# Performance work log

Measured on AMD Instinct MI355X. Metric: run time of the kernel, lower is better.

Reference implementation:

```python
import jax, jax.numpy as jnp
import numpy as np

N_NODES = 50000
N_EDGES = 600000
IN_DIM = 128
HID_DIM = 128


def setup_inputs() -> dict:
    key = jax.random.key(0)
    k_h, k_src, k_dst, k_w1, k_b1, k_w2, k_b2 = jax.random.split(key, 7)
    h = jax.random.normal(k_h, (N_NODES, IN_DIM), dtype=jnp.float32)
    src = jax.random.randint(k_src, (N_EDGES,), 0, N_NODES, dtype=jnp.int32)
    dst = jax.random.randint(k_dst, (N_EDGES,), 0, N_NODES, dtype=jnp.int32)
    # Edge MLP params: Linear(in_dim, out_dim) -> ReLU -> Linear(out_dim, 1) -> ReLU
    s1 = 1.0 / np.sqrt(IN_DIM)
    s2 = 1.0 / np.sqrt(HID_DIM)
    W1 = jax.random.uniform(k_w1, (IN_DIM, HID_DIM), jnp.float32, -s1, s1)
    b1 = jax.random.uniform(k_b1, (HID_DIM,), jnp.float32, -s1, s1)
    W2 = jax.random.uniform(k_w2, (HID_DIM, 1), jnp.float32, -s2, s2)
    b2 = jax.random.uniform(k_b2, (1,), jnp.float32, -s2, s2)
    return {"h": h, "src": src, "dst": dst, "W1": W1, "b1": b1, "W2": W2, "b2": b2}


def reference(h, src, dst, W1, b1, W2, b2):
    n_nodes = h.shape[0]
    # Edge MLP on feature differences (gather src/dst node features)
    dif = h[src] - h[dst]                                   # [E, D]
    hidden = jax.nn.relu(dif @ W1 + b1)                      # [E, H]
    att = jax.nn.relu(hidden @ W2 + b2)[:, 0]                # [E]
    att = jax.nn.sigmoid(att)                                # [E]
    # EdgeWeightNorm('right') on reversed graph: divide by the sum of
    # attention weights over edges sharing the same ORIGINAL source node.
    denom = jax.ops.segment_sum(att, src, num_segments=n_nodes)  # [N]
    w = att / denom[src]                                     # [E]
    # Message: w_e * src features, sum-aggregated at destination nodes
    msg = w[:, None] * h[src]                                # [E, D]
    out = jax.ops.segment_sum(msg, dst, num_segments=n_nodes)  # [N, D]
    return out
```

## Files before the change

### kernel.cpp

```cpp
#include <hip/hip_runtime.h>


typedef unsigned int uint;
typedef unsigned short ushort;
typedef __attribute__((ext_vector_type(8))) short short8;
typedef __attribute__((ext_vector_type(4))) float f32x4;

static __device__ __forceinline__ uint pack_f16(float a, float b) {
  _Float16 ha = (_Float16)a, hb = (_Float16)b;
  unsigned short ua = __builtin_bit_cast(unsigned short, ha);
  unsigned short ub = __builtin_bit_cast(unsigned short, hb);
  return ((uint)ub << 16) | ua;
}
static __device__ __forceinline__ float2 unpack_f16(uint u) {
  _Float16 lo = __builtin_bit_cast(_Float16, (unsigned short)(u & 0xffffu));
  _Float16 hi = __builtin_bit_cast(_Float16, (unsigned short)(u >> 16));
  return make_float2((float)lo, (float)hi);
}
static __device__ __forceinline__ ushort f2bf(float x) {
  uint u = __float_as_uint(x);
  u += 0x7fffu + ((u >> 16) & 1u);
  return (ushort)(u >> 16);
}

__global__ __launch_bounds__(256) void k_transpose(const float* __restrict__ W1,
                                                   ushort* __restrict__ w1t_swz) {
  int idx = blockIdx.x * 256 + threadIdx.x;
  int n = idx >> 7, k = idx & 127;
  float v = W1[k * 128 + n];
  int byte_off = n * 256 + ((k * 2) ^ ((n & 7) << 4));
  w1t_swz[byte_off >> 1] = f2bf(v);
}

__global__ __launch_bounds__(256) void k_gemm(const float* __restrict__ h,
                                              const ushort* __restrict__ w1t_swz,
                                              uint* __restrict__ gh,
                                              uint4* __restrict__ hh4,
                                              int n_nodes) {
  __shared__ ushort w1s[16384];
  int tid = threadIdx.x;
  {
    const uint4* srcw = (const uint4*)w1t_swz;
    uint4* dstw = (uint4*)w1s;
    #pragma unroll
    for (int i = 0; i < 8; ++i) dstw[tid + 256 * i] = srcw[tid + 256 * i];
  }
  __syncthreads();
  int wave = tid >> 6, lane = tid & 63;
  int tile = blockIdx.x * 4 + wave;
  if (tile * 16 >= n_nodes) return;
  int n0 = tile * 16;
  int l15 = lane & 15, kq = lane >> 4;
  int row = n0 + l15;

  f32x4 acc[8];
  #pragma unroll
  for (int ct = 0; ct < 8; ++ct) acc[ct] = (f32x4){0.f, 0.f, 0.f, 0.f};

  #pragma unroll
  for (int kb = 0; kb < 4; ++kb) {
    const float* hp = &h[(size_t)row * 128 + kb * 32 + kq * 8];
    float4 p0 = *(const float4*)hp;
    float4 p1 = *(const float4*)(hp + 4);
    short8 a;
    a[0] = (short)f2bf(p0.x); a[1] = (short)f2bf(p0.y);
    a[2] = (short)f2bf(p0.z); a[3] = (short)f2bf(p0.w);
    a[4] = (short)f2bf(p1.x); a[5] = (short)f2bf(p1.y);
    a[6] = (short)f2bf(p1.z); a[7] = (short)f2bf(p1.w);
    uint4 hv;
    hv.x = pack_f16(p0.x, p0.y); hv.y = pack_f16(p0.z, p0.w);
    hv.z = pack_f16(p1.x, p1.y); hv.w = pack_f16(p1.z, p1.w);
    hh4[(size_t)row * 16 + kb * 4 + kq] = hv;
    #pragma unroll
    for (int ct = 0; ct < 8; ++ct) {
      int n = ct * 16 + l15;
      int byte_off = n * 256 + (((kb * 64) + kq * 16) ^ ((n & 7) << 4));
      short8 b = *(const short8*)((const char*)w1s + byte_off);
      acc[ct] = __builtin_amdgcn_mfma_f32_16x16x32_bf16(a, b, acc[ct], 0, 0, 0);
    }
  }
  ushort* gh16 = (ushort*)gh;
  #pragma unroll
  for (int ct = 0; ct < 8; ++ct) {
    #pragma unroll
    for (int r = 0; r < 4; ++r) {
      int orow = n0 + kq * 4 + r;
      _Float16 v = (_Float16)acc[ct][r];
      gh16[(size_t)orow * 128 + ct * 16 + l15] = __builtin_bit_cast(unsigned short, v);
    }
  }
}

__global__ __launch_bounds__(256) void k_att(const uint4* __restrict__ gh4,
                                             const int* __restrict__ src,
                                             const int* __restrict__ dst,
                                             const float* __restrict__ b1,
                                             const float* __restrict__ W2,
                                             const float* __restrict__ b2,
                                             float* __restrict__ att,
                                             float* __restrict__ denom,
                                             int* __restrict__ counts,
                                             int n_edges) {
  int lane = threadIdx.x & 63;
  int sub = lane >> 4, l16 = lane & 15;
  int wid = (int)((blockIdx.x * blockDim.x + threadIdx.x) >> 6);
  int gw = (int)((gridDim.x * blockDim.x) >> 6);
  float4 b1a = *(const float4*)&b1[l16 * 8];
  float4 b1b = *(const float4*)&b1[l16 * 8 + 4];
  float4 w2a = *(const float4*)&W2[l16 * 8];
  float4 w2b = *(const float4*)&W2[l16 * 8 + 4];
  float b2v = b2[0];
  for (int e0 = wid * 4; e0 < n_edges; e0 += gw * 4) {
    int e = e0 + sub;
    bool valid = e < n_edges;
    int s = 0, d = 0;
    float acc = 0.f;
    if (valid) {
      s = src[e];
      d = dst[e];
      uint4 us = gh4[(size_t)s * 16 + l16];
      uint4 ud = gh4[(size_t)d * 16 + l16];
      float2 s0 = unpack_f16(us.x), s1 = unpack_f16(us.y);
      float2 s2 = unpack_f16(us.z), s3 = unpack_f16(us.w);
      float2 d0 = unpack_f16(ud.x), d1 = unpack_f16(ud.y);
      float2 d2 = unpack_f16(ud.z), d3 = unpack_f16(ud.w);
      float t;
      t = fmaxf(s0.x - d0.x + b1a.x, 0.f); acc = fmaf(t, w2a.x, acc);
      t = fmaxf(s0.y - d0.y + b1a.y, 0.f); acc = fmaf(t, w2a.y, acc);
      t = fmaxf(s1.x - d1.x + b1a.z, 0.f); acc = fmaf(t, w2a.z, acc);
      t = fmaxf(s1.y - d1.y + b1a.w, 0.f); acc = fmaf(t, w2a.w, acc);
      t = fmaxf(s2.x - d2.x + b1b.x, 0.f); acc = fmaf(t, w2b.x, acc);
      t = fmaxf(s2.y - d2.y + b1b.y, 0.f); acc = fmaf(t, w2b.y, acc);
      t = fmaxf(s3.x - d3.x + b1b.z, 0.f); acc = fmaf(t, w2b.z, acc);
      t = fmaxf(s3.y - d3.y + b1b.w, 0.f); acc = fmaf(t, w2b.w, acc);
    }
    acc += __shfl_xor(acc, 1);
    acc += __shfl_xor(acc, 2);
    acc += __shfl_xor(acc, 4);
    acc += __shfl_xor(acc, 8);
    if (l16 == 0 && valid) {
      float a = fmaxf(acc + b2v, 0.f);
      a = 1.f / (1.f + __expf(-a));
      att[e] = a;
      atomicAdd(&denom[s], a);
      atomicAdd(&counts[d], 1);
    }
  }
}

__global__ __launch_bounds__(256) void k_scanA(const int* __restrict__ counts,
                                               int* __restrict__ partials,
                                               int n, int chunk) {
  __shared__ int red[256];
  int b = blockIdx.x, t = threadIdx.x;
  int idx = b * chunk + t;
  red[t] = (t < chunk && idx < n) ? counts[idx] : 0;
  __syncthreads();
  for (int off = 128; off > 0; off >>= 1) {
    if (t < off) red[t] += red[t + off];
    __syncthreads();
  }
  if (t == 0) partials[b] = red[0];
}

__global__ __launch_bounds__(256) void k_scanB(int* __restrict__ partials,
                                               int* __restrict__ row_start,
                                               int n, int total) {
  __shared__ int p[256];
  int t = threadIdx.x;
  int orig = partials[t];
  p[t] = orig;
  __syncthreads();
  #pragma unroll
  for (int off = 1; off < 256; off <<= 1) {
    int v = (t >= off) ? p[t - off] : 0;
    __syncthreads();
    p[t] += v;
    __syncthreads();
  }
  partials[t] = p[t] - orig;
  if (t == 0) row_start[n] = total;
}

__global__ __launch_bounds__(256) void k_scanC(int* __restrict__ counts,
                                               const int* __restrict__ partials,
                                               int* __restrict__ row_start,
                                               int n, int chunk) {
  __shared__ int p[256];
  int b = blockIdx.x, t = threadIdx.x;
  int idx = b * chunk + t;
  bool ok = (t < chunk && idx < n);
  int orig = ok ? counts[idx] : 0;
  p[t] = orig;
  __syncthreads();
  #pragma unroll
  for (int off = 1; off < 256; off <<= 1) {
    int v = (t >= off) ? p[t - off] : 0;
    __syncthreads();
    p[t] += v;
    __syncthreads();
  }
  if (ok) {
    row_start[idx] = partials[b] + p[t] - orig;
    counts[idx] = 0;
  }
}

__global__ __launch_bounds__(256) void k_fill(const int* __restrict__ src,
                                              const int* __restrict__ dst,
                                              const float* __restrict__ att,
                                              const float* __restrict__ denom,
                                              const int* __restrict__ row_start,
                                              int* __restrict__ cursor,
                                              int2* __restrict__ bucket,
                                              int n_edges) {
  int i = blockIdx.x * blockDim.x + threadIdx.x;
  int stride = gridDim.x * blockDim.x;
  for (int e = i; e < n_edges; e += stride) {
    int d = dst[e], s = src[e];
    float w = att[e] / denom[s];
    int pos = atomicAdd(&cursor[d], 1);
    bucket[row_start[d] + pos] = make_int2(s, __float_as_int(w));
  }
}

__global__ __launch_bounds__(256) void k_agg(const uint4* __restrict__ hh4,
                                             const int* __restrict__ row_start,
                                             const int2* __restrict__ bucket,
                                             float* __restrict__ out, int n_nodes) {
  int lane = threadIdx.x & 63;
  int sub = lane >> 4, l16 = lane & 15;
  int d = blockIdx.x * 4 + (threadIdx.x >> 6);
  if (d >= n_nodes) return;
  int beg = row_start[d], end = row_start[d + 1];
  int cnt = end - beg;
  float a0 = 0.f, a1 = 0.f, a2 = 0.f, a3 = 0.f;
  float a4 = 0.f, a5 = 0.f, a6 = 0.f, a7 = 0.f;
  for (int base = 0; base < cnt; base += 64) {
    int nb = cnt - base; if (nb > 64) nb = 64;
    int2 ew = make_int2(0, 0);
    if (lane < nb) ew = bucket[beg + base + lane];
    int steps = (nb + 3) >> 2;
    for (int j = 0; j < steps; ++j) {
      int idx = j * 4 + sub;
      int s = __shfl(ew.x, idx);
      float w = __int_as_float(__shfl(ew.y, idx));
      if (idx < nb) {
        uint4 v = hh4[(size_t)s * 16 + l16];
        float2 f0 = unpack_f16(v.x), f1 = unpack_f16(v.y);
        float2 f2 = unpack_f16(v.z), f3 = unpack_f16(v.w);
        a0 = fmaf(w, f0.x, a0); a1 = fmaf(w, f0.y, a1);
        a2 = fmaf(w, f1.x, a2); a3 = fmaf(w, f1.y, a3);
        a4 = fmaf(w, f2.x, a4); a5 = fmaf(w, f2.y, a5);
        a6 = fmaf(w, f3.x, a6); a7 = fmaf(w, f3.y, a7);
      }
    }
  }
  #pragma unroll
  for (int off = 16; off < 64; off <<= 1) {
    a0 += __shfl_xor(a0, off); a1 += __shfl_xor(a1, off);
    a2 += __shfl_xor(a2, off); a3 += __shfl_xor(a3, off);
    a4 += __shfl_xor(a4, off); a5 += __shfl_xor(a5, off);
    a6 += __shfl_xor(a6, off); a7 += __shfl_xor(a7, off);
  }
  if (sub == 0) {
    *(float4*)&out[(size_t)d * 128 + l16 * 8]     = make_float4(a0, a1, a2, a3);
    *(float4*)&out[(size_t)d * 128 + l16 * 8 + 4] = make_float4(a4, a5, a6, a7);
  }
}

extern "C" void kernel_launch(void* const* d_in, const int* in_sizes, int n_in,
                              void* d_out, int out_size, void* d_ws, size_t ws_size,
                              hipStream_t stream) {
  const float* h   = (const float*)d_in[0];
  const int*   src = (const int*)d_in[1];
  const int*   dst = (const int*)d_in[2];
  const float* W1  = (const float*)d_in[3];
  const float* b1  = (const float*)d_in[4];
  const float* W2  = (const float*)d_in[5];
  const float* b2  = (const float*)d_in[6];
  float* out = (float*)d_out;

  int n_nodes = in_sizes[0] / 128;
  int n_edges = in_sizes[1];

  char* ws = (char*)d_ws;
  uint*   gh        = (uint*)ws;
  uint*   hh        = gh + (size_t)n_nodes * 64;
  float*  att       = (float*)(hh + (size_t)n_nodes * 64);
  float*  denom     = att + n_edges;
  int*    counts    = (int*)(denom + n_nodes);
  int*    row_start = counts + n_nodes;
  int*    partials  = row_start + n_nodes + 1;
  ushort* w1t       = (ushort*)(partials + 256);
  int2*   bucket    = (int2*)(((uintptr_t)(w1t + 16384) + 15) & ~(uintptr_t)15);

  hipMemsetAsync(denom, 0, (size_t)2 * n_nodes * sizeof(float), stream);

  int chunk = (n_nodes + 255) / 256;
  int n_tiles = (n_nodes + 15) / 16;
  k_transpose<<<64, 256, 0, stream>>>(W1, w1t);
  k_gemm <<<(n_tiles + 3) / 4, 256, 0, stream>>>(h, w1t, gh, (uint4*)hh, n_nodes);
  k_att  <<<2048, 256, 0, stream>>>((const uint4*)gh, src, dst, b1, W2, b2,
                                    att, denom, counts, n_edges);
  k_scanA<<<256, 256, 0, stream>>>(counts, partials, n_nodes, chunk);
  k_scanB<<<1, 256, 0, stream>>>(partials, row_start, n_nodes, n_edges);
  k_scanC<<<256, 256, 0, stream>>>(counts, partials, row_start, n_nodes, chunk);
  k_fill <<<2048, 256, 0, stream>>>(src, dst, att, denom, row_start, counts, bucket, n_edges);
  k_agg  <<<(n_nodes + 3) / 4, 256, 0, stream>>>((const uint4*)hh, row_start, bucket, out, n_nodes);
}
```

Before: 152.1 us.

## Compute edge attention in dst-sorted CSR order, reusing dst features per node

Builds the dst-bucketed CSR (histogram, scan, fill of source ids) before attention, then computes attention per destination node so the dst feature row and bias offsets are loaded once per node, not once per edge. Attention values go straight into the bucket array, and a separate pass then divides by the per-source denominator. This removes the per-edge dst gather and the att array round trip. It adds two extra launches (histogram and normalize) plus an extra pass over the bucket, and may load-imbalance on high-degree nodes.

```diff
diff --git a/kernel.cpp b/kernel.cpp
--- a/kernel.cpp
+++ b/kernel.cpp
@@ -91,61 +91,11 @@
   }
 }
 
-__global__ __launch_bounds__(256) void k_att(const uint4* __restrict__ gh4,
-                                             const int* __restrict__ src,
-                                             const int* __restrict__ dst,
-                                             const float* __restrict__ b1,
-                                             const float* __restrict__ W2,
-                                             const float* __restrict__ b2,
-                                             float* __restrict__ att,
-                                             float* __restrict__ denom,
-                                             int* __restrict__ counts,
-                                             int n_edges) {
-  int lane = threadIdx.x & 63;
-  int sub = lane >> 4, l16 = lane & 15;
-  int wid = (int)((blockIdx.x * blockDim.x + threadIdx.x) >> 6);
-  int gw = (int)((gridDim.x * blockDim.x) >> 6);
-  float4 b1a = *(const float4*)&b1[l16 * 8];
-  float4 b1b = *(const float4*)&b1[l16 * 8 + 4];
-  float4 w2a = *(const float4*)&W2[l16 * 8];
-  float4 w2b = *(const float4*)&W2[l16 * 8 + 4];
-  float b2v = b2[0];
-  for (int e0 = wid * 4; e0 < n_edges; e0 += gw * 4) {
-    int e = e0 + sub;
-    bool valid = e < n_edges;
-    int s = 0, d = 0;
-    float acc = 0.f;
-    if (valid) {
-      s = src[e];
-      d = dst[e];
-      uint4 us = gh4[(size_t)s * 16 + l16];
-      uint4 ud = gh4[(size_t)d * 16 + l16];
-      float2 s0 = unpack_f16(us.x), s1 = unpack_f16(us.y);
-      float2 s2 = unpack_f16(us.z), s3 = unpack_f16(us.w);
-      float2 d0 = unpack_f16(ud.x), d1 = unpack_f16(ud.y);
-      float2 d2 = unpack_f16(ud.z), d3 = unpack_f16(ud.w);
-      float t;
-      t = fmaxf(s0.x - d0.x + b1a.x, 0.f); acc = fmaf(t, w2a.x, acc);
-      t = fmaxf(s0.y - d0.y + b1a.y, 0.f); acc = fmaf(t, w2a.y, acc);
-      t = fmaxf(s1.x - d1.x + b1a.z, 0.f); acc = fmaf(t, w2a.z, acc);
-      t = fmaxf(s1.y - d1.y + b1a.w, 0.f); acc = fmaf(t, w2a.w, acc);
-      t = fmaxf(s2.x - d2.x + b1b.x, 0.f); acc = fmaf(t, w2b.x, acc);
-      t = fmaxf(s2.y - d2.y + b1b.y, 0.f); acc = fmaf(t, w2b.y, acc);
-      t = fmaxf(s3.x - d3.x + b1b.z, 0.f); acc = fmaf(t, w2b.z, acc);
-      t = fmaxf(s3.y - d3.y + b1b.w, 0.f); acc = fmaf(t, w2b.w, acc);
-    }
-    acc += __shfl_xor(acc, 1);
-    acc += __shfl_xor(acc, 2);
-    acc += __shfl_xor(acc, 4);
-    acc += __shfl_xor(acc, 8);
-    if (l16 == 0 && valid) {
-      float a = fmaxf(acc + b2v, 0.f);
-      a = 1.f / (1.f + __expf(-a));
-      att[e] = a;
-      atomicAdd(&denom[s], a);
-      atomicAdd(&counts[d], 1);
-    }
-  }
+__global__ __launch_bounds__(256) void k_hist(const int* __restrict__ dst,
+                                              int* __restrict__ counts, int n_edges) {
+  int i = blockIdx.x * blockDim.x + threadIdx.x;
+  int stride = gridDim.x * blockDim.x;
+  for (int e = i; e < n_edges; e += stride) atomicAdd(&counts[dst[e]], 1);
 }
 
 __global__ __launch_bounds__(256) void k_scanA(const int* __restrict__ counts,
@@ -206,21 +156,88 @@
   }
 }
 
-__global__ __launch_bounds__(256) void k_fill(const int* __restrict__ src,
-                                              const int* __restrict__ dst,
-                                              const float* __restrict__ att,
-                                              const float* __restrict__ denom,
-                                              const int* __restrict__ row_start,
-                                              int* __restrict__ cursor,
-                                              int2* __restrict__ bucket,
-                                              int n_edges) {
+__global__ __launch_bounds__(256) void k_fill0(const int* __restrict__ src,
+                                               const int* __restrict__ dst,
+                                               const int* __restrict__ row_start,
+                                               int* __restrict__ cursor,
+                                               int* __restrict__ bsrc,
+                                               int n_edges) {
   int i = blockIdx.x * blockDim.x + threadIdx.x;
   int stride = gridDim.x * blockDim.x;
   for (int e = i; e < n_edges; e += stride) {
-    int d = dst[e], s = src[e];
-    float w = att[e] / denom[s];
+    int d = dst[e];
     int pos = atomicAdd(&cursor[d], 1);
-    bucket[row_start[d] + pos] = make_int2(s, __float_as_int(w));
+    bsrc[row_start[d] + pos] = src[e];
+  }
+}
+
+__global__ __launch_bounds__(256) void k_att2(const uint4* __restrict__ gh4,
+                                              const int* __restrict__ bsrc,
+                                              const int* __restrict__ row_start,
+                                              const float* __restrict__ b1,
+                                              const float* __restrict__ W2,
+                                              const float* __restrict__ b2,
+                                              int2* __restrict__ bucket,
+                                              float* __restrict__ denom,
+                                              int n_nodes) {
+  int lane = threadIdx.x & 63;
+  int sub = lane >> 4, l16 = lane & 15;
+  int d = blockIdx.x * 4 + (threadIdx.x >> 6);
+  if (d >= n_nodes) return;
+  int beg = row_start[d], end = row_start[d + 1];
+  if (beg == end) return;
+  float4 b1a = *(const float4*)&b1[l16 * 8];
+  float4 b1b = *(const float4*)&b1[l16 * 8 + 4];
+  float4 w2a = *(const float4*)&W2[l16 * 8];
+  float4 w2b = *(const float4*)&W2[l16 * 8 + 4];
+  float b2v = b2[0];
+  uint4 ud = gh4[(size_t)d * 16 + l16];
+  float2 d0 = unpack_f16(ud.x), d1 = unpack_f16(ud.y);
+  float2 d2 = unpack_f16(ud.z), d3 = unpack_f16(ud.w);
+  float c0 = b1a.x - d0.x, c1 = b1a.y - d0.y, c2 = b1a.z - d1.x, c3 = b1a.w - d1.y;
+  float c4 = b1b.x - d2.x, c5 = b1b.y - d2.y, c6 = b1b.z - d3.x, c7 = b1b.w - d3.y;
+  for (int jb = beg; jb < end; jb += 4) {
+    int j = jb + sub;
+    bool valid = j < end;
+    int s = 0;
+    float acc = 0.f;
+    if (valid) {
+      s = bsrc[j];
+      uint4 us = gh4[(size_t)s * 16 + l16];
+      float2 s0 = unpack_f16(us.x), s1 = unpack_f16(us.y);
+      float2 s2 = unpack_f16(us.z), s3 = unpack_f16(us.w);
+      float t;
+      t = fmaxf(s0.x + c0, 0.f); acc = fmaf(t, w2a.x, acc);
+      t = fmaxf(s0.y + c1, 0.f); acc = fmaf(t, w2a.y, acc);
+      t = fmaxf(s1.x + c2, 0.f); acc = fmaf(t, w2a.z, acc);
+      t = fmaxf(s1.y + c3, 0.f); acc = fmaf(t, w2a.w, acc);
+      t = fmaxf(s2.x + c4, 0.f); acc = fmaf(t, w2b.x, acc);
+      t = fmaxf(s2.y + c5, 0.f); acc = fmaf(t, w2b.y, acc);
+      t = fmaxf(s3.x + c6, 0.f); acc = fmaf(t, w2b.z, acc);
+      t = fmaxf(s3.y + c7, 0.f); acc = fmaf(t, w2b.w, acc);
+    }
+    acc += __shfl_xor(acc, 1);
+    acc += __shfl_xor(acc, 2);
+    acc += __shfl_xor(acc, 4);
+    acc += __shfl_xor(acc, 8);
+    if (l16 == 0 && valid) {
+      float a = fmaxf(acc + b2v, 0.f);
+      a = 1.f / (1.f + __expf(-a));
+      bucket[j] = make_int2(s, __float_as_int(a));
+      atomicAdd(&denom[s], a);
+    }
+  }
+}
+
+__global__ __launch_bounds__(256) void k_w(int2* __restrict__ bucket,
+                                           const float* __restrict__ denom,
+                                           int n_edges) {
+  int i = blockIdx.x * blockDim.x + threadIdx.x;
+  int stride = gridDim.x * blockDim.x;
+  for (; i < n_edges; i += stride) {
+    int2 e = bucket[i];
+    float w = __int_as_float(e.y) / denom[e.x];
+    bucket[i] = make_int2(e.x, __float_as_int(w));
   }
 }
 
@@ -287,25 +304,28 @@
   char* ws = (char*)d_ws;
   uint*   gh        = (uint*)ws;
   uint*   hh        = gh + (size_t)n_nodes * 64;
-  float*  att       = (float*)(hh + (size_t)n_nodes * 64);
-  float*  denom     = att + n_edges;
+  float*  denom     = (float*)(hh + (size_t)n_nodes * 64);
   int*    counts    = (int*)(denom + n_nodes);
   int*    row_start = counts + n_nodes;
   int*    partials  = row_start + n_nodes + 1;
   ushort* w1t       = (ushort*)(partials + 256);
-  int2*   bucket    = (int2*)(((uintptr_t)(w1t + 16384) + 15) & ~(uintptr_t)15);
+  int*    bsrc      = (int*)(w1t + 16384);
+  int2*   bucket    = (int2*)(((uintptr_t)(bsrc + n_edges) + 15) & ~(uintptr_t)15);
 
   hipMemsetAsync(denom, 0, (size_t)2 * n_nodes * sizeof(float), stream);
 
   int chunk = (n_nodes + 255) / 256;
   int n_tiles = (n_nodes + 15) / 16;
+  int nblk4 = (n_nodes + 3) / 4;
   k_transpose<<<64, 256, 0, stream>>>(W1, w1t);
   k_gemm <<<(n_tiles + 3) / 4, 256, 0, stream>>>(h, w1t, gh, (uint4*)hh, n_nodes);
-  k_att  <<<2048, 256, 0, stream>>>((const uint4*)gh, src, dst, b1, W2, b2,
-                                    att, denom, counts, n_edges);
+  k_hist <<<1024, 256, 0, stream>>>(dst, counts, n_edges);
   k_scanA<<<256, 256, 0, stream>>>(counts, partials, n_nodes, chunk);
   k_scanB<<<1, 256, 0, stream>>>(partials, row_start, n_nodes, n_edges);
   k_scanC<<<256, 256, 0, stream>>>(counts, partials, row_start, n_nodes, chunk);
-  k_fill <<<2048, 256, 0, stream>>>(src, dst, att, denom, row_start, counts, bucket, n_edges);
-  k_agg  <<<(n_nodes + 3) / 4, 256, 0, stream>>>((const uint4*)hh, row_start, bucket, out, n_nodes);
-}
+  k_fill0<<<1024, 256, 0, stream>>>(src, dst, row_start, counts, bsrc, n_edges);
+  k_att2 <<<nblk4, 256, 0, stream>>>((const uint4*)gh, bsrc, row_start, b1, W2, b2,
+                                     bucket, denom, n_nodes);
+  k_w    <<<1024, 256, 0, stream>>>(bucket, denom, n_edges);
+  k_agg  <<<nblk4, 256, 0, stream>>>((const uint4*)hh, row_start, bucket, out, n_nodes);
+}
```

After: 166.3 us. 1.09x slower.
